# Optimization experiments

Hardware: AMD Instinct MI355X
Metric: run time of the kernel (lower is better)

The kernel has to match this reference:

```python
import jax, jax.numpy as jnp
import numpy as np

NUM_ENT, NUM_REL, ES = 100000, 200, 128
B, N, K = 4, 1024, 50  # batch of tasks, triples per task, max one-hop neighbors


def setup_inputs() -> dict:
    key = jax.random.key(0)
    ks = jax.random.split(key, 10)
    return {
        "ent_emb": jax.random.normal(ks[0], (NUM_ENT, ES), jnp.float32),
        "rel_emb": jax.random.normal(ks[1], (NUM_REL, ES), jnp.float32),
        "W_bil": jax.random.normal(ks[2], (ES, ES), jnp.float32) * 0.05,
        "W1": jax.random.normal(ks[3], (ES, ES), jnp.float32) * 0.05,
        "b1": jax.random.normal(ks[4], (ES,), jnp.float32) * 0.05,
        "W2": jax.random.normal(ks[5], (ES, ES), jnp.float32) * 0.05,
        "b2": jax.random.normal(ks[6], (ES,), jnp.float32) * 0.05,
        "head_idx": jax.random.randint(ks[7], (B, N), 0, NUM_ENT, jnp.int64),
        "tail_idx": jax.random.randint(ks[8], (B, N), 0, NUM_ENT, jnp.int64),
        "conn_rel": jax.random.randint(ks[9], (NUM_ENT, K), 0, NUM_REL, jnp.int64),
    }


def reference(ent_emb, rel_emb, W_bil, W1, b1, W2, b2, head_idx, tail_idx, conn_rel):
    # Gather head/tail entity embeddings: [B, N, es]
    h_e = ent_emb[head_idx]
    t_e = ent_emb[tail_idx]
    weak_rel = t_e - h_e  # weak relation signal, [B, N, es]

    # Gather one-hop relation embeddings of head/tail neighborhoods: [B, N, K, es]
    h_rel = rel_emb[conn_rel[head_idx]]
    t_rel = rel_emb[conn_rel[tail_idx]]

    # Bilinear score (out_features=1, no bias): score = x1 @ W @ x2
    ws = jnp.einsum('ij,bnj->bni', W_bil, weak_rel)       # [B, N, es]
    h_att = jax.nn.softmax(jnp.einsum('bnki,bni->bnk', h_rel, ws), axis=-1)
    t_att = jax.nn.softmax(jnp.einsum('bnki,bni->bnk', t_rel, ws), axis=-1)

    # Attention-weighted aggregate over neighbors: [B, N, es]
    head = jnp.einsum('bnk,bnki->bni', h_att, h_rel)
    tail = jnp.einsum('bnk,bnki->bni', t_att, t_rel)

    # Fused linear + relu (torch Linear: x @ W.T + b)
    h = jax.nn.relu(head @ W1.T + b1 + h_e @ W2.T + b2)
    t = jax.nn.relu(tail @ W1.T + b1 + t_e @ W2.T + b2)

    # cat along the singleton dim=2 -> [B, N, 2, es]
    return jnp.stack((h, t), axis=2)
```

## Files before the change

### kernel.cpp

```cpp
#include <hip/hip_runtime.h>

#define ES 128
#define KN 50

__device__ __forceinline__ unsigned short f32_to_bf16_rne(float f) {
    unsigned u = __float_as_uint(f);
    unsigned r = u + 0x7FFF + ((u >> 16) & 1);
    return (unsigned short)(r >> 16);
}
__device__ __forceinline__ float bf16_to_f32(unsigned short u) {
    return __uint_as_float(((unsigned)u) << 16);
}

__global__ __launch_bounds__(128) void prep_rwb(
    const float* __restrict__ rel, const float* __restrict__ Wb,
    float* __restrict__ rwb)
{
    const int r = blockIdx.x, j = threadIdx.x;
    float acc = 0.f;
    #pragma unroll 8
    for (int i = 0; i < ES; ++i)
        acc += rel[r * ES + i] * Wb[i * ES + j];
    rwb[r * ES + j] = acc;
}

__global__ __launch_bounds__(256) void prep_wtbf(
    const float* __restrict__ W1, const float* __restrict__ W2,
    unsigned short* __restrict__ wtb)
{
    int n = blockIdx.x * 256 + threadIdx.x;
    int j = n >> 7, c = n & 127;
    const float* src = (j < ES) ? W1 : W2;
    wtb[n] = f32_to_bf16_rne(src[c * ES + (j & 127)]);
}

#define LOADC(BUF, C) do {                                                   \
    _Pragma("unroll") for (int u = 0; u < 10; ++u) {                         \
        int k = (C) * 10 + u;                                                \
        int cid = (k < 32) ? cidA : cidB;                                    \
        int row = __shfl(cid, hb + (k & 31));                                \
        BUF[u] = *(const float4*)(RWb + (size_t)row * ES + 4 * q);           \
    } } while (0)

#define REDUCE(BUF, C) do {                                                  \
    float pv[10];                                                            \
    _Pragma("unroll") for (int u = 0; u < 10; ++u)                           \
        pv[u] = BUF[u].x*wr.x + BUF[u].y*wr.y + BUF[u].z*wr.z + BUF[u].w*wr.w;\
    _Pragma("unroll") for (int s = 1; s < 32; s <<= 1)                       \
        { _Pragma("unroll") for (int u = 0; u < 10; ++u)                     \
            pv[u] += __shfl_xor(pv[u], s); }                                 \
    _Pragma("unroll") for (int u = 0; u < 10; ++u) {                         \
        int k = (C) * 10 + u;                                                \
        if (k < 32) s1 = (q == k)      ? pv[u] : s1;                         \
        else        s2 = (q == k - 32) ? pv[u] : s2;                         \
    } } while (0)

#define XADD(a) do { a.x += __shfl_xor(a.x, 32); a.y += __shfl_xor(a.y, 32); \
                     a.z += __shfl_xor(a.z, 32); a.w += __shfl_xor(a.w, 32); } while (0)

__global__ __launch_bounds__(128, 4) void onehop_main(
    const float* __restrict__ ent, const float* __restrict__ rel,
    const float* __restrict__ b1, const float* __restrict__ b2,
    const int* __restrict__ hidx, const int* __restrict__ tidx,
    const int* __restrict__ conn,
    const float* __restrict__ RWb, const unsigned short* __restrict__ WTB,
    float* __restrict__ out, int npair, int num_ent, int num_rel)
{
    __shared__ float coef[4][2 * ES];
    __shared__ float part[2][4][ES];

    const int tid  = threadIdx.x;
    const int wave = tid >> 6;
    const int lane = tid & 63;
    const int q    = lane & 31;
    const int hi   = lane >> 5;
    const int hb   = lane & 32;

    const int pair = min(blockIdx.x * 2 + wave, npair - 1);

    int hid = min(max(hidx[pair], 0), num_ent - 1);
    int tdi = min(max(tidx[pair], 0), num_ent - 1);

    float4 he = *(const float4*)(ent + (size_t)hid * ES + 4 * q);
    float4 te = *(const float4*)(ent + (size_t)tdi * ES + 4 * q);
    float4 wr;
    wr.x = te.x - he.x; wr.y = te.y - he.y;
    wr.z = te.z - he.z; wr.w = te.w - he.w;
    *(float4*)(&coef[2 * wave + hi][ES + 4 * q]) = hi ? te : he;

    const int cl = min(lane, KN - 1);
    int ch = min(max(conn[(size_t)hid * KN + cl], 0), num_rel - 1);
    int ct = min(max(conn[(size_t)tdi * KN + cl], 0), num_rel - 1);
    int ctq  = __shfl(ct, q);
    int cidA = hi ? ctq : ch;
    int cB_l = __shfl(ch, q + 32);
    int cB_h = __shfl(ct, q + 32);
    int cidB = hi ? cB_h : cB_l;

    float s1 = -1e30f, s2 = -1e30f;
    {
        float4 bufA[10], bufB[10];
        LOADC(bufA, 0); LOADC(bufB, 1);
        REDUCE(bufA, 0); LOADC(bufA, 2);
        REDUCE(bufB, 1); LOADC(bufB, 3);
        REDUCE(bufA, 2); LOADC(bufA, 4);
        REDUCE(bufB, 3);
        REDUCE(bufA, 4);
    }

    float m = fmaxf(s1, s2);
    #pragma unroll
    for (int s = 1; s < 32; s <<= 1) m = fmaxf(m, __shfl_xor(m, s));
    float e1 = __expf(s1 - m), e2 = __expf(s2 - m);
    float l = e1 + e2;
    #pragma unroll
    for (int s = 1; s < 32; s <<= 1) l += __shfl_xor(l, s);
    float rinv = 1.f / l;
    e1 *= rinv; e2 *= rinv;

    float4 agg = {0.f, 0.f, 0.f, 0.f};
    #pragma unroll 10
    for (int k = 0; k < KN; ++k) {
        int src = hb + (k & 31);
        float ev = __shfl((k < 32) ? e1 : e2, src);
        int row  = __shfl((k < 32) ? cidA : cidB, src);
        float4 v = *(const float4*)(rel + (size_t)row * ES + 4 * q);
        agg.x += ev * v.x; agg.y += ev * v.y;
        agg.z += ev * v.z; agg.w += ev * v.w;
    }
    *(float4*)(&coef[2 * wave + hi][4 * q]) = agg;
    __syncthreads();

    const int jbase = wave << 7;
    float4 a0 = {0,0,0,0}, a1 = {0,0,0,0}, a2 = {0,0,0,0}, a3 = {0,0,0,0};
    #pragma unroll 8
    for (int jj = 0; jj < 64; ++jj) {
        int j0 = jbase + 2 * jj;
        ushort4 wv = *(const ushort4*)(WTB + (size_t)j0 * ES + 4 * lane);
        float w0 = bf16_to_f32(wv.x), w1 = bf16_to_f32(wv.y);
        float w2 = bf16_to_f32(wv.z), w3 = bf16_to_f32(wv.w);
        int jl = j0 + hi;
        float c0 = coef[0][jl], c1 = coef[1][jl];
        float c2 = coef[2][jl], c3 = coef[3][jl];
        a0.x += c0*w0; a0.y += c0*w1; a0.z += c0*w2; a0.w += c0*w3;
        a1.x += c1*w0; a1.y += c1*w1; a1.z += c1*w2; a1.w += c1*w3;
        a2.x += c2*w0; a2.y += c2*w1; a2.z += c2*w2; a2.w += c2*w3;
        a3.x += c3*w0; a3.y += c3*w1; a3.z += c3*w2; a3.w += c3*w3;
    }
    XADD(a0); XADD(a1); XADD(a2); XADD(a3);
    if (!hi) {
        *(float4*)(&part[wave][0][4 * q]) = a0;
        *(float4*)(&part[wave][1][4 * q]) = a1;
        *(float4*)(&part[wave][2][4 * q]) = a2;
        *(float4*)(&part[wave][3][4 * q]) = a3;
    }
    __syncthreads();

    const int o = tid >> 5, q2 = tid & 31;
    float4 p0 = *(const float4*)(&part[0][o][4 * q2]);
    float4 p1 = *(const float4*)(&part[1][o][4 * q2]);
    float4 v1 = *(const float4*)(b1 + 4 * q2);
    float4 v2 = *(const float4*)(b2 + 4 * q2);
    float4 r;
    r.x = fmaxf(p0.x + p1.x + v1.x + v2.x, 0.f);
    r.y = fmaxf(p0.y + p1.y + v1.y + v2.y, 0.f);
    r.z = fmaxf(p0.z + p1.z + v1.z + v2.z, 0.f);
    r.w = fmaxf(p0.w + p1.w + v1.w + v2.w, 0.f);
    const int orow = blockIdx.x * 4 + o;
    if (orow < 2 * npair)
        *(float4*)(out + (size_t)orow * ES + 4 * q2) = r;
}

extern "C" void kernel_launch(void* const* d_in, const int* in_sizes, int n_in,
                              void* d_out, int out_size, void* d_ws, size_t ws_size,
                              hipStream_t stream) {
    const float* ent = (const float*)d_in[0];
    const float* rel = (const float*)d_in[1];
    const float* Wb  = (const float*)d_in[2];
    const float* W1  = (const float*)d_in[3];
    const float* b1  = (const float*)d_in[4];
    const float* W2  = (const float*)d_in[5];
    const float* b2  = (const float*)d_in[6];
    const int* hidx  = (const int*)d_in[7];
    const int* tidx  = (const int*)d_in[8];
    const int* conn  = (const int*)d_in[9];
    float* out = (float*)d_out;

    const int npair   = in_sizes[7];
    const int num_ent = in_sizes[0] / ES;
    const int num_rel = in_sizes[1] / ES;

    float* rwb = (float*)d_ws;
    unsigned short* wtb = (unsigned short*)(rwb + (size_t)num_rel * ES);

    prep_rwb<<<num_rel, 128, 0, stream>>>(rel, Wb, rwb);
    prep_wtbf<<<(2 * ES * ES) / 256, 256, 0, stream>>>(W1, W2, wtb);

    const int nblocks = (npair + 1) / 2;
    onehop_main<<<nblocks, 128, 0, stream>>>(
        ent, rel, b1, b2, hidx, tidx, conn,
        rwb, wtb, out, npair, num_ent, num_rel);
}
```

Measured before the change: 146.7 us.

## Split each pair's head and tail attention across separate waves

Blocks grow from 128 to 256 threads: each wave now handles only one side (head or tail) of a pair, and each half-wave takes 25 of the 50 neighbors. The half-wave aggregates are summed with a cross-half shuffle. The output projection is split across four waves, each covering 64 input features, with a four-way LDS reduction. This doubles thread-level parallelism and roughly halves per-thread register work, which should help hide gather latency. The cost is recomputing the shared embedding loads per wave and adding extra shuffles and LDS traffic.

New measurement: 156.6 us. +6.7%, slower.

```diff
diff --git a/kernel.cpp b/kernel.cpp
--- a/kernel.cpp
+++ b/kernel.cpp
@@ -35,30 +35,26 @@
 }
 
 #define LOADC(BUF, C) do {                                                   \
-    _Pragma("unroll") for (int u = 0; u < 10; ++u) {                         \
-        int k = (C) * 10 + u;                                                \
-        int cid = (k < 32) ? cidA : cidB;                                    \
-        int row = __shfl(cid, hb + (k & 31));                                \
+    _Pragma("unroll") for (int u = 0; u < 5; ++u) {                          \
+        int row = __shfl(cid, hb + 5 * (C) + u);                             \
         BUF[u] = *(const float4*)(RWb + (size_t)row * ES + 4 * q);           \
     } } while (0)
 
 #define REDUCE(BUF, C) do {                                                  \
-    float pv[10];                                                            \
-    _Pragma("unroll") for (int u = 0; u < 10; ++u)                           \
+    float pv[5];                                                             \
+    _Pragma("unroll") for (int u = 0; u < 5; ++u)                            \
         pv[u] = BUF[u].x*wr.x + BUF[u].y*wr.y + BUF[u].z*wr.z + BUF[u].w*wr.w;\
     _Pragma("unroll") for (int s = 1; s < 32; s <<= 1)                       \
-        { _Pragma("unroll") for (int u = 0; u < 10; ++u)                     \
+        { _Pragma("unroll") for (int u = 0; u < 5; ++u)                      \
             pv[u] += __shfl_xor(pv[u], s); }                                 \
-    _Pragma("unroll") for (int u = 0; u < 10; ++u) {                         \
-        int k = (C) * 10 + u;                                                \
-        if (k < 32) s1 = (q == k)      ? pv[u] : s1;                         \
-        else        s2 = (q == k - 32) ? pv[u] : s2;                         \
-    } } while (0)
+    _Pragma("unroll") for (int u = 0; u < 5; ++u)                            \
+        s1 = (q == 5 * (C) + u) ? pv[u] : s1;                                \
+    } while (0)
 
 #define XADD(a) do { a.x += __shfl_xor(a.x, 32); a.y += __shfl_xor(a.y, 32); \
                      a.z += __shfl_xor(a.z, 32); a.w += __shfl_xor(a.w, 32); } while (0)
 
-__global__ __launch_bounds__(128, 4) void onehop_main(
+__global__ __launch_bounds__(256, 8) void onehop_main(
     const float* __restrict__ ent, const float* __restrict__ rel,
     const float* __restrict__ b1, const float* __restrict__ b2,
     const int* __restrict__ hidx, const int* __restrict__ tidx,
@@ -67,39 +63,35 @@
     float* __restrict__ out, int npair, int num_ent, int num_rel)
 {
     __shared__ float coef[4][2 * ES];
-    __shared__ float part[2][4][ES];
+    __shared__ float part[4][4][ES];
 
     const int tid  = threadIdx.x;
-    const int wave = tid >> 6;
+    const int w    = tid >> 6;
     const int lane = tid & 63;
     const int q    = lane & 31;
     const int hi   = lane >> 5;
     const int hb   = lane & 32;
 
-    const int pair = min(blockIdx.x * 2 + wave, npair - 1);
+    const int pair = min(blockIdx.x * 2 + (w >> 1), npair - 1);
+    const int side = w & 1;
 
     int hid = min(max(hidx[pair], 0), num_ent - 1);
     int tdi = min(max(tidx[pair], 0), num_ent - 1);
+    int eid = side ? tdi : hid;
 
     float4 he = *(const float4*)(ent + (size_t)hid * ES + 4 * q);
     float4 te = *(const float4*)(ent + (size_t)tdi * ES + 4 * q);
     float4 wr;
     wr.x = te.x - he.x; wr.y = te.y - he.y;
     wr.z = te.z - he.z; wr.w = te.w - he.w;
-    *(float4*)(&coef[2 * wave + hi][ES + 4 * q]) = hi ? te : he;
+    if (!hi) *(float4*)(&coef[w][ES + 4 * q]) = side ? te : he;
 
-    const int cl = min(lane, KN - 1);
-    int ch = min(max(conn[(size_t)hid * KN + cl], 0), num_rel - 1);
-    int ct = min(max(conn[(size_t)tdi * KN + cl], 0), num_rel - 1);
-    int ctq  = __shfl(ct, q);
-    int cidA = hi ? ctq : ch;
-    int cB_l = __shfl(ch, q + 32);
-    int cB_h = __shfl(ct, q + 32);
-    int cidB = hi ? cB_h : cB_l;
+    const int kl  = 25 * hi + min(q, 24);
+    int cid = min(max(conn[(size_t)eid * KN + kl], 0), num_rel - 1);
 
-    float s1 = -1e30f, s2 = -1e30f;
+    float s1 = -1e30f;
     {
-        float4 bufA[10], bufB[10];
+        float4 bufA[5], bufB[5];
         LOADC(bufA, 0); LOADC(bufB, 1);
         REDUCE(bufA, 0); LOADC(bufA, 2);
         REDUCE(bufB, 1); LOADC(bufB, 3);
@@ -108,33 +100,33 @@
         REDUCE(bufA, 4);
     }
 
-    float m = fmaxf(s1, s2);
+    float m = s1;
     #pragma unroll
-    for (int s = 1; s < 32; s <<= 1) m = fmaxf(m, __shfl_xor(m, s));
-    float e1 = __expf(s1 - m), e2 = __expf(s2 - m);
-    float l = e1 + e2;
+    for (int s = 1; s < 64; s <<= 1) m = fmaxf(m, __shfl_xor(m, s));
+    float e1 = __expf(s1 - m);
+    float l = e1;
     #pragma unroll
-    for (int s = 1; s < 32; s <<= 1) l += __shfl_xor(l, s);
-    float rinv = 1.f / l;
-    e1 *= rinv; e2 *= rinv;
+    for (int s = 1; s < 64; s <<= 1) l += __shfl_xor(l, s);
+    e1 *= (1.f / l);
 
     float4 agg = {0.f, 0.f, 0.f, 0.f};
-    #pragma unroll 10
-    for (int k = 0; k < KN; ++k) {
-        int src = hb + (k & 31);
-        float ev = __shfl((k < 32) ? e1 : e2, src);
-        int row  = __shfl((k < 32) ? cidA : cidB, src);
+    #pragma unroll 5
+    for (int t = 0; t < 25; ++t) {
+        int src  = hb + t;
+        float ev = __shfl(e1, src);
+        int row  = __shfl(cid, src);
         float4 v = *(const float4*)(rel + (size_t)row * ES + 4 * q);
         agg.x += ev * v.x; agg.y += ev * v.y;
         agg.z += ev * v.z; agg.w += ev * v.w;
     }
-    *(float4*)(&coef[2 * wave + hi][4 * q]) = agg;
+    XADD(agg);
+    if (!hi) *(float4*)(&coef[w][4 * q]) = agg;
     __syncthreads();
 
-    const int jbase = wave << 7;
+    const int jbase = w << 6;
     float4 a0 = {0,0,0,0}, a1 = {0,0,0,0}, a2 = {0,0,0,0}, a3 = {0,0,0,0};
     #pragma unroll 8
-    for (int jj = 0; jj < 64; ++jj) {
+    for (int jj = 0; jj < 32; ++jj) {
         int j0 = jbase + 2 * jj;
         ushort4 wv = *(const ushort4*)(WTB + (size_t)j0 * ES + 4 * lane);
         float w0 = bf16_to_f32(wv.x), w1 = bf16_to_f32(wv.y);
@@ -149,26 +141,27 @@
     }
     XADD(a0); XADD(a1); XADD(a2); XADD(a3);
     if (!hi) {
-        *(float4*)(&part[wave][0][4 * q]) = a0;
-        *(float4*)(&part[wave][1][4 * q]) = a1;
-        *(float4*)(&part[wave][2][4 * q]) = a2;
-        *(float4*)(&part[wave][3][4 * q]) = a3;
+        *(float4*)(&part[w][0][4 * q]) = a0;
+        *(float4*)(&part[w][1][4 * q]) = a1;
+        *(float4*)(&part[w][2][4 * q]) = a2;
+        *(float4*)(&part[w][3][4 * q]) = a3;
     }
     __syncthreads();
 
-    const int o = tid >> 5, q2 = tid & 31;
-    float4 p0 = *(const float4*)(&part[0][o][4 * q2]);
-    float4 p1 = *(const float4*)(&part[1][o][4 * q2]);
-    float4 v1 = *(const float4*)(b1 + 4 * q2);
-    float4 v2 = *(const float4*)(b2 + 4 * q2);
-    float4 r;
-    r.x = fmaxf(p0.x + p1.x + v1.x + v2.x, 0.f);
-    r.y = fmaxf(p0.y + p1.y + v1.y + v2.y, 0.f);
-    r.z = fmaxf(p0.z + p1.z + v1.z + v2.z, 0.f);
-    r.w = fmaxf(p0.w + p1.w + v1.w + v2.w, 0.f);
-    const int orow = blockIdx.x * 4 + o;
-    if (orow < 2 * npair)
-        *(float4*)(out + (size_t)orow * ES + 4 * q2) = r;
+    const int o = tid >> 6, c2i = tid & 63;
+    float px = part[0][o][2*c2i]     + part[1][o][2*c2i]
+             + part[2][o][2*c2i]     + part[3][o][2*c2i];
+    float py = part[0][o][2*c2i + 1] + part[1][o][2*c2i + 1]
+             + part[2][o][2*c2i + 1] + part[3][o][2*c2i + 1];
+    float bx = b1[2*c2i]     + b2[2*c2i];
+    float by = b1[2*c2i + 1] + b2[2*c2i + 1];
+    const int opair = blockIdx.x * 2 + (o >> 1);
+    if (opair < npair) {
+        float2 r;
+        r.x = fmaxf(px + bx, 0.f);
+        r.y = fmaxf(py + by, 0.f);
+        *(float2*)(out + (size_t)(opair * 2 + (o & 1)) * ES + 2 * c2i) = r;
+    }
 }
 
 extern "C" void kernel_launch(void* const* d_in, const int* in_sizes, int n_in,
@@ -197,7 +190,7 @@
     prep_wtbf<<<(2 * ES * ES) / 256, 256, 0, stream>>>(W1, W2, wtb);
 
     const int nblocks = (npair + 1) / 2;
-    onehop_main<<<nblocks, 128, 0, stream>>>(
+    onehop_main<<<nblocks, 256, 0, stream>>>(
         ent, rel, b1, b2, hidx, tidx, conn,
         rwb, wtb, out, npair, num_ent, num_rel);
 }
```
